# Performance work log

Hardware: AMD Instinct MI355X
Metric: run time of the kernel (lower is better)

## Reference

```python
import jax, jax.numpy as jnp
import numpy as np

IN_DIM = 4096
OUT_DIM = 4096
CODEBOOK_SIZE = 65536
LAYER_ID = 3
HASH_A, HASH_B, HASH_C = 10007, 20011, 40009
SIGN_HASH_A, SIGN_HASH_B, SIGN_HASH_C = 4099, 6151, 14887
SIGNED_HASH = True
BATCH = 8192


def _hash_tables():
    i = jnp.arange(OUT_DIM, dtype=jnp.int64 if jax.config.jax_enable_x64 else jnp.int32)[:, None]
    j = jnp.arange(IN_DIM, dtype=i.dtype)[None, :]
    idx = (i * HASH_A + j * HASH_B + LAYER_ID * HASH_C) % CODEBOOK_SIZE
    bits = (i * SIGN_HASH_A + j * SIGN_HASH_B + LAYER_ID * SIGN_HASH_C) % 2
    signs = bits.astype(jnp.float32) * 2.0 - 1.0
    return idx, signs


def setup_inputs() -> dict:
    key = jax.random.key(0)
    kx, kc = jax.random.split(key)
    x = jax.random.normal(kx, (BATCH, IN_DIM), dtype=jnp.float32)
    codebook = jax.random.normal(kc, (CODEBOOK_SIZE,), dtype=jnp.float32) * 0.01
    bias = jnp.zeros((OUT_DIM,), dtype=jnp.float32)
    return {"x": x, "codebook": codebook, "bias": bias}


def reference(x, codebook, bias):
    idx, signs = _hash_tables()  # [out_dim, in_dim] each
    weight = codebook[idx]  # gather from tiny codebook -> [out_dim, in_dim]
    if SIGNED_HASH:
        weight = weight * signs.astype(weight.dtype)
    # F.linear: y = x @ W^T + b
    return jnp.einsum('bi,oi->bo', x, weight) + bias
```

## Files before the change

### kernel.cpp

```cpp
#include <hip/hip_runtime.h>
#include <hip/hip_bf16.h>

constexpr int M_ = 8192;
constexpr int N_ = 4096;
constexpr int K_ = 4096;
constexpr int CBOOK = 65536;
constexpr int HA = 10007, HB = 20011;
constexpr int HC3 = 3 * 40009;

constexpr int BM = 256, BN = 128, BK = 64;
constexpr int KITERS = K_ / BK;

using bf16x8 = __bf16 __attribute__((ext_vector_type(8)));
using f32x4  = float __attribute__((ext_vector_type(4)));
using u16x8  = unsigned short __attribute__((ext_vector_type(8)));

typedef __attribute__((address_space(3))) void lds_void_t;
typedef const __attribute__((address_space(1))) void gbl_void_t;

static __device__ __forceinline__ unsigned short f2bf(float f) {
    __bf16 h = (__bf16)f;
    return __builtin_bit_cast(unsigned short, h);
}

constexpr int GENB  = N_ * K_ / 8 / 256;
constexpr int CONVB = M_ * K_ / 8 / 256;

__global__ __launch_bounds__(256) void prep_kernel(const float* __restrict__ x,
                                                   const float* __restrict__ cb,
                                                   unsigned short* __restrict__ Wf,
                                                   unsigned short* __restrict__ xb) {
    const int b = blockIdx.x;
    if (b < GENB) {
        const int t     = b * 256 + threadIdx.x;
        const int lane  = t & 63;
        const int ktile = (t >> 6) & 127;
        const int ntile = t >> 13;
        const int n  = (ntile << 4) + (lane & 15);
        const int kb = (ktile << 5) + ((lane >> 4) << 3);
        const int h  = n * HA + kb * HB + HC3;
        u16x8 out;
#pragma unroll
        for (int j = 0; j < 8; ++j) {
            const int idx = (h + j * HB) & (CBOOK - 1);
            float v = cb[idx];
            v = ((n ^ (kb + j)) & 1) ? -v : v;
            out[j] = f2bf(v);
        }
        *reinterpret_cast<u16x8*>(&Wf[(size_t)t * 8]) = out;
    } else {
        const size_t t = (size_t)(b - GENB) * 256 + threadIdx.x;
        const float4* p = reinterpret_cast<const float4*>(x) + t * 2;
        const float4 a = p[0], c = p[1];
        u16x8 out;
        out[0] = f2bf(a.x); out[1] = f2bf(a.y); out[2] = f2bf(a.z); out[3] = f2bf(a.w);
        out[4] = f2bf(c.x); out[5] = f2bf(c.y); out[6] = f2bf(c.z); out[7] = f2bf(c.w);
        reinterpret_cast<u16x8*>(xb)[t] = out;
    }
}

__global__ __launch_bounds__(256, 2) void gemm_kernel(
        const unsigned short* __restrict__ A,
        const unsigned short* __restrict__ Wf,
        const float* __restrict__ bias,
        float* __restrict__ C) {
    __shared__ __align__(16) unsigned short ldsA[2][BM * BK];

    const int tid  = threadIdx.x;
    const int lane = tid & 63;
    const int wv   = tid >> 6;
    const int m0 = blockIdx.y * BM;
    const int n0 = blockIdx.x * BN;

    const int quad = lane >> 4;
    const int l16  = lane & 15;
    const int lr = lane >> 3;
    const int lc = lane & 7;
    const int scol = (lc ^ lr) * 8;
    const int sw   = l16 & 7;

    const unsigned short* aLane = A + (size_t)(m0 + lr) * K_ + scol;
    const unsigned short* wLane = Wf + (size_t)lane * 8;
    const int ntile0 = n0 >> 4;

    f32x4 acc[4][8] = {};

#pragma unroll
    for (int r = 0; r < 8; ++r) {
        const int rowb = wv * 64 + r * 8;
        __builtin_amdgcn_global_load_lds(
            (gbl_void_t*)(aLane + (size_t)rowb * K_),
            (lds_void_t*)&ldsA[0][rowb * BK], 16, 0, 0);
    }

    for (int i = 0; i < KITERS; ++i) {
        __syncthreads();
        const int buf = i & 1;

        if (i + 1 < KITERS) {
            const unsigned short* aNext = aLane + (size_t)(i + 1) * BK;
#pragma unroll
            for (int r = 0; r < 8; ++r) {
                const int rowb = wv * 64 + r * 8;
                __builtin_amdgcn_global_load_lds(
                    (gbl_void_t*)(aNext + (size_t)rowb * K_),
                    (lds_void_t*)&ldsA[buf ^ 1][rowb * BK], 16, 0, 0);
            }
        }

        bf16x8 bfr[2][8];
#pragma unroll
        for (int kk = 0; kk < 2; ++kk)
#pragma unroll
            for (int nt = 0; nt < 8; ++nt)
                bfr[kk][nt] = *reinterpret_cast<const bf16x8*>(
                    wLane + (((size_t)(ntile0 + nt) << 7) + i * 2 + kk) * 512);

#pragma unroll
        for (int kk = 0; kk < 2; ++kk) {
            bf16x8 af[4];
            const int blk = ((kk * 4 + quad) ^ sw) * 8;
#pragma unroll
            for (int mt = 0; mt < 4; ++mt)
                af[mt] = *reinterpret_cast<const bf16x8*>(
                    &ldsA[buf][(wv * 64 + mt * 16 + l16) * BK + blk]);
#pragma unroll
            for (int mt = 0; mt < 4; ++mt)
#pragma unroll
                for (int nt = 0; nt < 8; ++nt)
                    acc[mt][nt] = __builtin_amdgcn_mfma_f32_16x16x32_bf16(
                        af[mt], bfr[kk][nt], acc[mt][nt], 0, 0, 0);
        }
    }

#pragma unroll
    for (int nt = 0; nt < 8; ++nt) {
        const int col = n0 + nt * 16 + l16;
        const float bv = bias[col];
#pragma unroll
        for (int mt = 0; mt < 4; ++mt) {
            const int rowb = m0 + wv * 64 + mt * 16 + quad * 4;
#pragma unroll
            for (int r = 0; r < 4; ++r)
                C[(size_t)(rowb + r) * N_ + col] = acc[mt][nt][r] + bv;
        }
    }
}

__global__ __launch_bounds__(256) void naive_kernel(const float* __restrict__ x,
                                                    const float* __restrict__ cb,
                                                    const float* __restrict__ bias,
                                                    float* __restrict__ out) {
    const size_t t = (size_t)blockIdx.x * 256 + threadIdx.x;
    const int row = (int)(t / N_);
    const int col = (int)(t % N_);
    float s = bias[col];
    const float* xr = x + (size_t)row * K_;
    const int h = col * HA + HC3;
    for (int i = 0; i < K_; ++i) {
        float v = cb[(h + i * HB) & (CBOOK - 1)];
        s += xr[i] * (((col ^ i) & 1) ? -v : v);
    }
    out[t] = s;
}

extern "C" void kernel_launch(void* const* d_in, const int* in_sizes, int n_in,
                              void* d_out, int out_size, void* d_ws, size_t ws_size,
                              hipStream_t stream) {
    const float* x    = (const float*)d_in[0];
    const float* cb   = (const float*)d_in[1];
    const float* bias = (const float*)d_in[2];
    float* out = (float*)d_out;

    const size_t wBytes = (size_t)N_ * K_ * sizeof(unsigned short);
    const size_t xBytes = (size_t)M_ * K_ * sizeof(unsigned short);

    if (ws_size >= wBytes + xBytes) {
        unsigned short* Wf = (unsigned short*)d_ws;
        unsigned short* xb = (unsigned short*)((char*)d_ws + wBytes);
        prep_kernel<<<GENB + CONVB, 256, 0, stream>>>(x, cb, Wf, xb);
        gemm_kernel<<<dim3(N_ / BN, M_ / BM), 256, 0, stream>>>(xb, Wf, bias, out);
    } else {
        naive_kernel<<<(int)((size_t)M_ * N_ / 256), 256, 0, stream>>>(x, cb, bias, out);
    }
}
```

Measured before the change: 524.5 us.

## Replace materialized hashed weight matrix with compact shifted signed-codebook table

Because HA ≡ 197·HB (mod 65536), every weight W[n][k] equals entry C0·n+k of a single 1-D signed, permuted codebook sequence. The change therefore builds 8 copies of that sequence, each shifted by one element so 16-byte loads stay aligned, about 1.1 MB in total, instead of the full 32 MB bf16 weight matrix. The GEMM indexes B fragments through per-column offsets into this table. This removes most of the weight-generation prep work and lets B reads hit in cache, at the cost of scattered, less coalesced 16-byte B loads.

```diff
diff --git a/kernel.cpp b/kernel.cpp
--- a/kernel.cpp
+++ b/kernel.cpp
@@ -7,6 +7,8 @@
 constexpr int CBOOK = 65536;
 constexpr int HA = 10007, HB = 20011;
 constexpr int HC3 = 3 * 40009;
+
+constexpr int C0 = 197;
 
 constexpr int BM = 256, BN = 128, BK = 64;
 constexpr int KITERS = K_ / BK;
@@ -23,33 +25,28 @@
     return __builtin_bit_cast(unsigned short, h);
 }
 
-constexpr int GENB  = N_ * K_ / 8 / 256;
+constexpr int PADE  = 69640;
+constexpr int PTOT  = 8 * PADE;
+constexpr int PB    = (PTOT + 255) / 256;
 constexpr int CONVB = M_ * K_ / 8 / 256;
 
 __global__ __launch_bounds__(256) void prep_kernel(const float* __restrict__ x,
                                                    const float* __restrict__ cb,
-                                                   unsigned short* __restrict__ Wf,
+                                                   unsigned short* __restrict__ P2p,
                                                    unsigned short* __restrict__ xb) {
     const int b = blockIdx.x;
-    if (b < GENB) {
-        const int t     = b * 256 + threadIdx.x;
-        const int lane  = t & 63;
-        const int ktile = (t >> 6) & 127;
-        const int ntile = t >> 13;
-        const int n  = (ntile << 4) + (lane & 15);
-        const int kb = (ktile << 5) + ((lane >> 4) << 3);
-        const int h  = n * HA + kb * HB + HC3;
-        u16x8 out;
-#pragma unroll
-        for (int j = 0; j < 8; ++j) {
-            const int idx = (h + j * HB) & (CBOOK - 1);
-            float v = cb[idx];
-            v = ((n ^ (kb + j)) & 1) ? -v : v;
-            out[j] = f2bf(v);
+    if (b < PB) {
+        const int t = b * 256 + threadIdx.x;
+        if (t < PTOT) {
+            const int p = t / PADE;
+            const int i = t - p * PADE;
+            const int u = i + p;
+            float v = cb[(u * HB + HC3) & (CBOOK - 1)];
+            if (u & 1) v = -v;
+            P2p[t] = f2bf(v);
         }
-        *reinterpret_cast<u16x8*>(&Wf[(size_t)t * 8]) = out;
     } else {
-        const size_t t = (size_t)(b - GENB) * 256 + threadIdx.x;
+        const size_t t = (size_t)(b - PB) * 256 + threadIdx.x;
         const float4* p = reinterpret_cast<const float4*>(x) + t * 2;
         const float4 a = p[0], c = p[1];
         u16x8 out;
@@ -61,7 +58,7 @@
 
 __global__ __launch_bounds__(256, 2) void gemm_kernel(
         const unsigned short* __restrict__ A,
-        const unsigned short* __restrict__ Wf,
+        const unsigned short* __restrict__ P2p,
         const float* __restrict__ bias,
         float* __restrict__ C) {
     __shared__ __align__(16) unsigned short ldsA[2][BM * BK];
@@ -80,8 +77,16 @@
     const int sw   = l16 & 7;
 
     const unsigned short* aLane = A + (size_t)(m0 + lr) * K_ + scol;
-    const unsigned short* wLane = Wf + (size_t)lane * 8;
+    const char* p2b = reinterpret_cast<const char*>(P2p);
     const int ntile0 = n0 >> 4;
+
+    int boff[8];
+#pragma unroll
+    for (int nt = 0; nt < 8; ++nt) {
+        const int n = ((ntile0 + nt) << 4) + l16;
+        const int e = (C0 * n) & (CBOOK - 1);
+        boff[nt] = ((e & 7) * PADE + ((e >> 3) << 3) + quad * 8) * 2;
+    }
 
     f32x4 acc[4][8] = {};
 
@@ -114,7 +119,7 @@
 #pragma unroll
             for (int nt = 0; nt < 8; ++nt)
                 bfr[kk][nt] = *reinterpret_cast<const bf16x8*>(
-                    wLane + (((size_t)(ntile0 + nt) << 7) + i * 2 + kk) * 512);
+                    p2b + boff[nt] + (i * 64 + kk * 32) * 2);
 
 #pragma unroll
         for (int kk = 0; kk < 2; ++kk) {
@@ -172,14 +177,14 @@
     const float* bias = (const float*)d_in[2];
     float* out = (float*)d_out;
 
-    const size_t wBytes = (size_t)N_ * K_ * sizeof(unsigned short);
+    const size_t pBytes = (size_t)PTOT * sizeof(unsigned short);
     const size_t xBytes = (size_t)M_ * K_ * sizeof(unsigned short);
 
-    if (ws_size >= wBytes + xBytes) {
-        unsigned short* Wf = (unsigned short*)d_ws;
-        unsigned short* xb = (unsigned short*)((char*)d_ws + wBytes);
-        prep_kernel<<<GENB + CONVB, 256, 0, stream>>>(x, cb, Wf, xb);
-        gemm_kernel<<<dim3(N_ / BN, M_ / BM), 256, 0, stream>>>(xb, Wf, bias, out);
+    if (ws_size >= pBytes + xBytes) {
+        unsigned short* P2p = (unsigned short*)d_ws;
+        unsigned short* xb  = (unsigned short*)((char*)d_ws + pBytes);
+        prep_kernel<<<PB + CONVB, 256, 0, stream>>>(x, cb, P2p, xb);
+        gemm_kernel<<<dim3(N_ / BN, M_ / BM), 256, 0, stream>>>(xb, P2p, bias, out);
     } else {
         naive_kernel<<<(int)((size_t)M_ * N_ / 256), 256, 0, stream>>>(x, cb, bias, out);
     }
```

Result: slower. 655.7 us (+25.0%).

## Stage both operands through LDS with a 256x256 tile and triple buffering

Applied to the files above, without the earlier changes.

The GEMM now uses 512 threads and a 256x256 block tile with BK=32. Both the activation and weight tiles are staged into LDS through a three-deep global_load_lds pipeline, using explicit waitcnt and barrier calls and a higher MFMA issue priority. The prep kernel writes weights in a swizzled per-N-block layout that matches the new LDS layout. The aim is to stop each wave reloading weight fragments straight from global memory and to raise operand reuse per block, in exchange for more LDS use and register pressure.

```diff
diff --git a/kernel.cpp b/kernel.cpp
--- a/kernel.cpp
+++ b/kernel.cpp
@@ -8,8 +8,8 @@
 constexpr int HA = 10007, HB = 20011;
 constexpr int HC3 = 3 * 40009;
 
-constexpr int BM = 256, BN = 128, BK = 64;
-constexpr int KITERS = K_ / BK;
+constexpr int BM = 256, BN = 256, BK = 32;
+constexpr int NKT = K_ / BK;
 
 using bf16x8 = __bf16 __attribute__((ext_vector_type(8)));
 using f32x4  = float __attribute__((ext_vector_type(4)));
@@ -32,19 +32,21 @@
                                                    unsigned short* __restrict__ xb) {
     const int b = blockIdx.x;
     if (b < GENB) {
-        const int t     = b * 256 + threadIdx.x;
-        const int lane  = t & 63;
-        const int ktile = (t >> 6) & 127;
-        const int ntile = t >> 13;
-        const int n  = (ntile << 4) + (lane & 15);
-        const int kb = (ktile << 5) + ((lane >> 4) << 3);
-        const int h  = n * HA + kb * HB + HC3;
+        const int t    = b * 256 + threadIdx.x;
+        const int slot = t & 1023;
+        const int kt   = (t >> 10) & 127;
+        const int nb   = t >> 17;
+        const int row  = slot >> 2;
+        const int key  = (row >> 1) & 3;
+        const int n  = (nb << 8) + row;
+        const int k0 = (kt << 5) + (((slot & 3) ^ key) << 3);
+        const int h  = n * HA + k0 * HB + HC3;
         u16x8 out;
 #pragma unroll
         for (int j = 0; j < 8; ++j) {
             const int idx = (h + j * HB) & (CBOOK - 1);
             float v = cb[idx];
-            v = ((n ^ (kb + j)) & 1) ? -v : v;
+            v = ((n ^ (k0 + j)) & 1) ? -v : v;
             out[j] = f2bf(v);
         }
         *reinterpret_cast<u16x8*>(&Wf[(size_t)t * 8]) = out;
@@ -59,87 +61,93 @@
     }
 }
 
-__global__ __launch_bounds__(256, 2) void gemm_kernel(
+__global__ __launch_bounds__(512, 2) void gemm_kernel(
         const unsigned short* __restrict__ A,
         const unsigned short* __restrict__ Wf,
         const float* __restrict__ bias,
         float* __restrict__ C) {
-    __shared__ __align__(16) unsigned short ldsA[2][BM * BK];
+    __shared__ __align__(16) unsigned short sm[3 * 8192 * 2];
+    unsigned short* As = sm;
+    unsigned short* Bs = sm + 3 * 8192;
 
     const int tid  = threadIdx.x;
     const int lane = tid & 63;
-    const int wv   = tid >> 6;
+    const int w    = tid >> 6;
+    const int wm   = w >> 2;
+    const int wn   = w & 3;
     const int m0 = blockIdx.y * BM;
     const int n0 = blockIdx.x * BN;
 
     const int quad = lane >> 4;
     const int l16  = lane & 15;
-    const int lr = lane >> 3;
-    const int lc = lane & 7;
-    const int scol = (lc ^ lr) * 8;
-    const int sw   = l16 & 7;
 
-    const unsigned short* aLane = A + (size_t)(m0 + lr) * K_ + scol;
-    const unsigned short* wLane = Wf + (size_t)lane * 8;
-    const int ntile0 = n0 >> 4;
+    const int sblk = (lane & 3) ^ ((lane >> 3) & 3);
+    const unsigned short* aLane =
+        A + (size_t)(m0 + w * 16 + (lane >> 2)) * K_ + sblk * 8;
+    const unsigned short* bLane =
+        Wf + (size_t)blockIdx.x * NKT * 8192 + tid * 8;
 
-    f32x4 acc[4][8] = {};
+    const int rblk = (quad ^ ((l16 >> 1) & 3)) * 8;
+    const unsigned short* aRd = As + (wm * 128 + l16) * 32 + rblk;
+    const unsigned short* bRd = Bs + (wn * 64 + l16) * 32 + rblk;
 
+    f32x4 acc[8][4] = {};
+
+    auto STAGE = [&](int kt, int bs) {
 #pragma unroll
-    for (int r = 0; r < 8; ++r) {
-        const int rowb = wv * 64 + r * 8;
-        __builtin_amdgcn_global_load_lds(
-            (gbl_void_t*)(aLane + (size_t)rowb * K_),
-            (lds_void_t*)&ldsA[0][rowb * BK], 16, 0, 0);
-    }
+        for (int r = 0; r < 2; ++r) {
+            __builtin_amdgcn_global_load_lds(
+                (gbl_void_t*)(aLane + (size_t)r * 128 * K_ + (size_t)kt * BK),
+                (lds_void_t*)(As + bs * 8192 + (r * 512 + w * 64) * 8), 16, 0, 0);
+            __builtin_amdgcn_global_load_lds(
+                (gbl_void_t*)(bLane + (size_t)kt * 8192 + r * 4096),
+                (lds_void_t*)(Bs + bs * 8192 + (r * 512 + w * 64) * 8), 16, 0, 0);
+        }
+    };
 
-    for (int i = 0; i < KITERS; ++i) {
-        __syncthreads();
-        const int buf = i & 1;
+    STAGE(0, 0);
+    STAGE(1, 1);
 
-        if (i + 1 < KITERS) {
-            const unsigned short* aNext = aLane + (size_t)(i + 1) * BK;
-#pragma unroll
-            for (int r = 0; r < 8; ++r) {
-                const int rowb = wv * 64 + r * 8;
-                __builtin_amdgcn_global_load_lds(
-                    (gbl_void_t*)(aNext + (size_t)rowb * K_),
-                    (lds_void_t*)&ldsA[buf ^ 1][rowb * BK], 16, 0, 0);
-            }
+    int bC = 0;
+    for (int kt = 0; kt < NKT; ++kt) {
+        asm volatile("s_waitcnt lgkmcnt(0)" ::: "memory");
+        if (kt < NKT - 1) asm volatile("s_waitcnt vmcnt(4)" ::: "memory");
+        else              asm volatile("s_waitcnt vmcnt(0)" ::: "memory");
+        __builtin_amdgcn_s_barrier();
+        __builtin_amdgcn_sched_barrier(0);
+
+        if (kt + 2 < NKT) {
+            int bS = bC + 2; if (bS >= 3) bS -= 3;
+            STAGE(kt + 2, bS);
         }
 
-        bf16x8 bfr[2][8];
+        bf16x8 bfr[4], afr[8];
 #pragma unroll
-        for (int kk = 0; kk < 2; ++kk)
+        for (int nt = 0; nt < 4; ++nt)
+            bfr[nt] = *reinterpret_cast<const bf16x8*>(bRd + bC * 8192 + nt * 512);
 #pragma unroll
-            for (int nt = 0; nt < 8; ++nt)
-                bfr[kk][nt] = *reinterpret_cast<const bf16x8*>(
-                    wLane + (((size_t)(ntile0 + nt) << 7) + i * 2 + kk) * 512);
+        for (int mt = 0; mt < 8; ++mt)
+            afr[mt] = *reinterpret_cast<const bf16x8*>(aRd + bC * 8192 + mt * 512);
 
+        __builtin_amdgcn_s_setprio(1);
 #pragma unroll
-        for (int kk = 0; kk < 2; ++kk) {
-            bf16x8 af[4];
-            const int blk = ((kk * 4 + quad) ^ sw) * 8;
+        for (int mt = 0; mt < 8; ++mt)
 #pragma unroll
-            for (int mt = 0; mt < 4; ++mt)
-                af[mt] = *reinterpret_cast<const bf16x8*>(
-                    &ldsA[buf][(wv * 64 + mt * 16 + l16) * BK + blk]);
-#pragma unroll
-            for (int mt = 0; mt < 4; ++mt)
-#pragma unroll
-                for (int nt = 0; nt < 8; ++nt)
-                    acc[mt][nt] = __builtin_amdgcn_mfma_f32_16x16x32_bf16(
-                        af[mt], bfr[kk][nt], acc[mt][nt], 0, 0, 0);
-        }
+            for (int nt = 0; nt < 4; ++nt)
+                acc[mt][nt] = __builtin_amdgcn_mfma_f32_16x16x32_bf16(
+                    afr[mt], bfr[nt], acc[mt][nt], 0, 0, 0);
+        __builtin_amdgcn_s_setprio(0);
+
+        ++bC; if (bC == 3) bC = 0;
     }
 
 #pragma unroll
-    for (int nt = 0; nt < 8; ++nt) {
-        const int col = n0 + nt * 16 + l16;
+    for (int nt = 0; nt < 4; ++nt) {
+        const int col = n0 + wn * 64 + nt * 16 + l16;
         const float bv = bias[col];
 #pragma unroll
-        for (int mt = 0; mt < 4; ++mt) {
-            const int rowb = m0 + wv * 64 + mt * 16 + quad * 4;
+        for (int mt = 0; mt < 8; ++mt) {
+            const int rowb = m0 + wm * 128 + mt * 16 + quad * 4;
 #pragma unroll
             for (int r = 0; r < 4; ++r)
                 C[(size_t)(rowb + r) * N_ + col] = acc[mt][nt][r] + bv;
@@ -179,7 +187,7 @@
         unsigned short* Wf = (unsigned short*)d_ws;
         unsigned short* xb = (unsigned short*)((char*)d_ws + wBytes);
         prep_kernel<<<GENB + CONVB, 256, 0, stream>>>(x, cb, Wf, xb);
-        gemm_kernel<<<dim3(N_ / BN, M_ / BM), 256, 0, stream>>>(xb, Wf, bias, out);
+        gemm_kernel<<<dim3(N_ / BN, M_ / BM), 512, 0, stream>>>(xb, Wf, bias, out);
     } else {
         naive_kernel<<<(int)((size_t)M_ * N_ / 256), 256, 0, stream>>>(x, cb, bias, out);
     }
```

Measured after the change: 463.1 us. 11.7% less time.
